# Kernel optimization log

Measured on AMD Instinct MI355X. Metric: run time of the kernel, lower is better.

The kernel has to match this reference:

```python
import jax, jax.numpy as jnp
import numpy as np

B, IN, H = 32768, 256, 256
CONCAT = IN + H

def _xavier(key, shape):
    fan_in, fan_out = shape
    limit = float(np.sqrt(6.0 / (fan_in + fan_out)))
    return jax.random.uniform(key, shape, jnp.float32, -limit, limit)

def setup_inputs() -> dict:
    key = jax.random.key(0)
    k = jax.random.split(key, 6)
    return {
        "x": jax.random.normal(k[0], (B, 1, IN), jnp.float32),
        "h_prev": jax.random.normal(k[1], (B, 1, H), jnp.float32),
        "wr": _xavier(k[2], (CONCAT, H)),
        "wz": _xavier(k[3], (CONCAT, H)),
        "whh": _xavier(k[4], (H, H)),
        "whx": _xavier(k[5], (IN, H)),
        "br": jnp.zeros((H,), jnp.float32),
        "bz": jnp.zeros((H,), jnp.float32),
        "bh": jnp.zeros((H,), jnp.float32),
    }

def reference(x, h_prev, wr, wz, whh, whx, br, bz, bh):
    # x: [B,1,IN], h_prev: [B,1,H]
    xc = jnp.concatenate([x, h_prev], axis=2)                  # [B,1,IN+H]
    r = jax.nn.sigmoid(jnp.matmul(xc, wr) + br)                # reset gate
    z = jax.nn.sigmoid(jnp.matmul(xc, wz) + bz)                # update gate
    g = jnp.tanh(jnp.matmul(r * h_prev, whh) + jnp.matmul(x, whx) + bh)
    h = (1 - z) * h_prev + z * g                               # gated blend
    return h
```

## Files before the change

### kernel.cpp

```cpp
#include <hip/hip_runtime.h>
#include <hip/hip_bf16.h>
#include <stdint.h>


typedef float  f32x4  __attribute__((ext_vector_type(4)));
typedef __bf16 bf16x8 __attribute__((ext_vector_type(8)));
typedef short  s16x8  __attribute__((ext_vector_type(8)));

#define B_TOT   32768
#define MT      64
#define WRZ_ELEMS (512*512)
#define WG_ELEMS  (256*512)

__device__ __forceinline__ unsigned short f2b(float f) {
    union { float f; unsigned int u; } v; v.f = f;
    unsigned int r = (v.u + 0x7FFFu + ((v.u >> 16) & 1u)) >> 16;
    return (unsigned short)r;
}
__device__ __forceinline__ float b2f(unsigned short b) {
    union { unsigned int u; float f; } v; v.u = ((unsigned int)b) << 16;
    return v.f;
}
__device__ __forceinline__ ushort2 pk2(float a, float b) {
    __hip_bfloat162 t = __float22bfloat162_rn(make_float2(a, b));
    union { __hip_bfloat162 h; ushort2 u; } c; c.h = t; return c.u;
}
__device__ __forceinline__ float sigmoid_f(float x) {
    return 1.0f / (1.0f + __expf(-x));
}
__device__ __forceinline__ float tanh_f(float x) {
    return 1.0f - 2.0f / (__expf(2.0f * x) + 1.0f);
}

__device__ __forceinline__ int lds_idx(int row, int col) {
    return row * 512 + ((((col >> 3) ^ (row & 7)) << 3) | (col & 7));
}

__global__ void prep_weights(const float* __restrict__ wr,
                             const float* __restrict__ wz,
                             const float* __restrict__ whh,
                             const float* __restrict__ whx,
                             unsigned short* __restrict__ wrz,
                             unsigned short* __restrict__ wg) {
    const int b = blockIdx.x;
    const int t = threadIdx.x;
    union { s16x8 v; unsigned short u[8]; } tmp;

    if (b < 128) {
        int w = b >> 4, ks = b & 15;
        int jn = t >> 6, l = t & 63;
        int kbase = ks * 32 + ((l >> 4) << 3);
        int n = 32 * w + ((jn & 1) << 4) + (l & 15);
        const float* src = (jn < 2) ? wr : wz;
        #pragma unroll
        for (int jj = 0; jj < 8; ++jj)
            tmp.u[jj] = f2b(src[(kbase + jj) * 256 + n]);
        *reinterpret_cast<s16x8*>(wrz + (size_t)w * 32768 + ks * 2048 + t * 8) = tmp.v;
    } else {
        int b2 = b - 128;
        int w = b2 >> 3, ksp = b2 & 7;
        int ksl = t >> 7, j = (t >> 6) & 1, l = t & 63;
        int ks = ksp * 2 + ksl;
        int kbase = ks * 32 + ((l >> 4) << 3);
        int n = 32 * w + (j << 4) + (l & 15);
        #pragma unroll
        for (int jj = 0; jj < 8; ++jj) {
            int k = kbase + jj;
            tmp.u[jj] = f2b((k < 256) ? whx[k * 256 + n] : whh[(k - 256) * 256 + n]);
        }
        *reinterpret_cast<s16x8*>(wg + (size_t)w * 16384 + ksp * 2048 + t * 8) = tmp.v;
    }
}

__global__ __launch_bounds__(512, 2)
void gru_fused(const float* __restrict__ x, const float* __restrict__ h,
               const unsigned short* __restrict__ wrz,
               const unsigned short* __restrict__ wg,
               const float* __restrict__ br, const float* __restrict__ bz,
               const float* __restrict__ bh, float* __restrict__ out) {
    __shared__ unsigned short xcA[64 * 512];

    const int tid  = threadIdx.x;
    const int lane = tid & 63;
    const int wv   = tid >> 6;
    const int m0   = lane & 15;
    const int q    = lane >> 4;
    const int rowBase = blockIdx.x * MT;

    float brv[2], bzv[2], bhv[2];
    #pragma unroll
    for (int j = 0; j < 2; ++j) {
        int col = 32 * wv + j * 16 + m0;
        brv[j] = br[col]; bzv[j] = bz[col]; bhv[j] = bh[col];
    }

    #pragma unroll
    for (int it = 0; it < 8; ++it) {
        int row = it * 8 + wv;
        size_t g = (size_t)(rowBase + row) * 256 + lane * 4;
        float4 xv = *reinterpret_cast<const float4*>(x + g);
        float4 hv = *reinterpret_cast<const float4*>(h + g);
        ushort2 x0 = pk2(xv.x, xv.y), x1 = pk2(xv.z, xv.w);
        ushort2 h0 = pk2(hv.x, hv.y), h1 = pk2(hv.z, hv.w);
        ushort4 xb = make_ushort4(x0.x, x0.y, x1.x, x1.y);
        ushort4 hb = make_ushort4(h0.x, h0.y, h1.x, h1.y);
        *reinterpret_cast<ushort4*>(&xcA[lds_idx(row, lane * 4)])       = xb;
        *reinterpret_cast<ushort4*>(&xcA[lds_idx(row, 256 + lane * 4)]) = hb;
    }

    const unsigned short* wrzP = wrz + (size_t)wv * 32768;
    const unsigned short* wgP  = wg  + (size_t)wv * 16384;

    s16x8 Bb[2][12];
    #pragma unroll
    for (int k2 = 0; k2 < 2; ++k2) {
        #pragma unroll
        for (int jn = 0; jn < 4; ++jn)
            Bb[0][k2 * 6 + jn] = *reinterpret_cast<const s16x8*>(
                wrzP + k2 * 2048 + jn * 512 + lane * 8);
        #pragma unroll
        for (int j = 0; j < 2; ++j)
            Bb[0][k2 * 6 + 4 + j] = *reinterpret_cast<const s16x8*>(
                wgP + k2 * 1024 + j * 512 + lane * 8);
    }

    __syncthreads();

    f32x4 rz[4][4];
    f32x4 gac[2][4];
    #pragma unroll
    for (int jn = 0; jn < 4; ++jn)
        #pragma unroll
        for (int mt = 0; mt < 4; ++mt)
            rz[jn][mt] = (f32x4){0.f, 0.f, 0.f, 0.f};
    #pragma unroll
    for (int j = 0; j < 2; ++j)
        #pragma unroll
        for (int mt = 0; mt < 4; ++mt)
            gac[j][mt] = (f32x4){0.f, 0.f, 0.f, 0.f};

    #pragma unroll
    for (int grp = 0; grp < 8; ++grp) {
        const int cur = grp & 1, nxt = cur ^ 1;
        if (grp < 7) {
            int gn = grp + 1;
            #pragma unroll
            for (int k2 = 0; k2 < 2; ++k2) {
                int ks = gn * 2 + k2;
                #pragma unroll
                for (int jn = 0; jn < 4; ++jn)
                    Bb[nxt][k2 * 6 + jn] = *reinterpret_cast<const s16x8*>(
                        wrzP + ks * 2048 + jn * 512 + lane * 8);
                if (gn < 4) {
                    #pragma unroll
                    for (int j = 0; j < 2; ++j)
                        Bb[nxt][k2 * 6 + 4 + j] = *reinterpret_cast<const s16x8*>(
                            wgP + ks * 1024 + j * 512 + lane * 8);
                }
            }
        }
        __builtin_amdgcn_sched_barrier(0);
        #pragma unroll
        for (int k2 = 0; k2 < 2; ++k2) {
            int ks = grp * 2 + k2;
            bf16x8 afr[4];
            #pragma unroll
            for (int mt = 0; mt < 4; ++mt) {
                int row = mt * 16 + m0;
                int idx = row * 512 + ((((ks << 2) | q) ^ (row & 7)) << 3);
                afr[mt] = __builtin_bit_cast(bf16x8,
                    *reinterpret_cast<const s16x8*>(&xcA[idx]));
            }
            #pragma unroll
            for (int jn = 0; jn < 4; ++jn) {
                bf16x8 bf = __builtin_bit_cast(bf16x8, Bb[cur][k2 * 6 + jn]);
                #pragma unroll
                for (int mt = 0; mt < 4; ++mt)
                    rz[jn][mt] = __builtin_amdgcn_mfma_f32_16x16x32_bf16(
                        afr[mt], bf, rz[jn][mt], 0, 0, 0);
            }
            if (grp < 4) {
                #pragma unroll
                for (int j = 0; j < 2; ++j) {
                    bf16x8 bf = __builtin_bit_cast(bf16x8, Bb[cur][k2 * 6 + 4 + j]);
                    #pragma unroll
                    for (int mt = 0; mt < 4; ++mt)
                        gac[j][mt] = __builtin_amdgcn_mfma_f32_16x16x32_bf16(
                            afr[mt], bf, gac[j][mt], 0, 0, 0);
                }
            }
        }
    }
    __syncthreads();

    s16x8 Tb[2][4];
    #pragma unroll
    for (int k2 = 0; k2 < 2; ++k2)
        #pragma unroll
        for (int j = 0; j < 2; ++j)
            Tb[0][k2 * 2 + j] = *reinterpret_cast<const s16x8*>(
                wgP + (8 + k2) * 1024 + j * 512 + lane * 8);

    #pragma unroll
    for (int j = 0; j < 2; ++j) {
        int col = 32 * wv + j * 16 + m0;
        #pragma unroll
        for (int mt = 0; mt < 4; ++mt) {
            #pragma unroll
            for (int rg = 0; rg < 4; ++rg) {
                int row = mt * 16 + q * 4 + rg;
                float hval = b2f(xcA[lds_idx(row, 256 + col)]);
                float rs = sigmoid_f(rz[j][mt][rg] + brv[j]);
                xcA[lds_idx(row, col)] = f2b(rs * hval);
                rz[j][mt][rg] = hval;
            }
        }
    }
    __syncthreads();

    #pragma unroll
    for (int tg = 0; tg < 4; ++tg) {
        const int cur = tg & 1, nxt = cur ^ 1;
        if (tg < 3) {
            #pragma unroll
            for (int k2 = 0; k2 < 2; ++k2)
                #pragma unroll
                for (int j = 0; j < 2; ++j)
                    Tb[nxt][k2 * 2 + j] = *reinterpret_cast<const s16x8*>(
                        wgP + (10 + tg * 2 + k2) * 1024 + j * 512 + lane * 8);
        }
        __builtin_amdgcn_sched_barrier(0);
        #pragma unroll
        for (int k2 = 0; k2 < 2; ++k2) {
            int kt = tg * 2 + k2;
            bf16x8 afr[4];
            #pragma unroll
            for (int mt = 0; mt < 4; ++mt) {
                int row = mt * 16 + m0;
                int idx = row * 512 + ((((kt << 2) | q) ^ (row & 7)) << 3);
                afr[mt] = __builtin_bit_cast(bf16x8,
                    *reinterpret_cast<const s16x8*>(&xcA[idx]));
            }
            #pragma unroll
            for (int j = 0; j < 2; ++j) {
                bf16x8 bf = __builtin_bit_cast(bf16x8, Tb[cur][k2 * 2 + j]);
                #pragma unroll
                for (int mt = 0; mt < 4; ++mt)
                    gac[j][mt] = __builtin_amdgcn_mfma_f32_16x16x32_bf16(
                        afr[mt], bf, gac[j][mt], 0, 0, 0);
            }
        }
    }

    #pragma unroll
    for (int j = 0; j < 2; ++j) {
        int col = 32 * wv + j * 16 + m0;
        #pragma unroll
        for (int mt = 0; mt < 4; ++mt) {
            #pragma unroll
            for (int rg = 0; rg < 4; ++rg) {
                int row = mt * 16 + q * 4 + rg;
                float zs = sigmoid_f(rz[2 + j][mt][rg] + bzv[j]);
                float gv = tanh_f(gac[j][mt][rg] + bhv[j]);
                float hval = rz[j][mt][rg];
                out[(size_t)(rowBase + row) * 256 + col] = hval + zs * (gv - hval);
            }
        }
    }
}

extern "C" void kernel_launch(void* const* d_in, const int* in_sizes, int n_in,
                              void* d_out, int out_size, void* d_ws, size_t ws_size,
                              hipStream_t stream) {
    const float* x   = (const float*)d_in[0];
    const float* h   = (const float*)d_in[1];
    const float* wr  = (const float*)d_in[2];
    const float* wz  = (const float*)d_in[3];
    const float* whh = (const float*)d_in[4];
    const float* whx = (const float*)d_in[5];
    const float* br  = (const float*)d_in[6];
    const float* bz  = (const float*)d_in[7];
    const float* bh  = (const float*)d_in[8];
    float* out = (float*)d_out;

    unsigned short* wrz = (unsigned short*)d_ws;
    unsigned short* wg  = wrz + WRZ_ELEMS;

    prep_weights<<<192, 256, 0, stream>>>(wr, wz, whh, whx, wrz, wg);
    gru_fused<<<B_TOT / MT, 512, 0, stream>>>(x, h, wrz, wg, br, bz, bh, out);
}
```

Measured before the change: 145.6 us.

## Stream activation tiles into LDS per k-group overlapped with MFMA compute

```diff
diff --git a/kernel.cpp b/kernel.cpp
--- a/kernel.cpp
+++ b/kernel.cpp
@@ -34,6 +34,13 @@
 
 __device__ __forceinline__ int lds_idx(int row, int col) {
     return row * 512 + ((((col >> 3) ^ (row & 7)) << 3) | (col & 7));
+}
+
+__device__ __forceinline__ void stash8(unsigned short* dst, float4 a, float4 b) {
+    union { ushort2 u2[4]; s16x8 v; } pk;
+    pk.u2[0] = pk2(a.x, a.y); pk.u2[1] = pk2(a.z, a.w);
+    pk.u2[2] = pk2(b.x, b.y); pk.u2[3] = pk2(b.z, b.w);
+    *reinterpret_cast<s16x8*>(dst) = pk.v;
 }
 
 __global__ void prep_weights(const float* __restrict__ wr,
@@ -72,7 +79,7 @@
     }
 }
 
-__global__ __launch_bounds__(512, 2)
+__global__ __launch_bounds__(512, 4)
 void gru_fused(const float* __restrict__ x, const float* __restrict__ h,
                const unsigned short* __restrict__ wrz,
                const unsigned short* __restrict__ wg,
@@ -94,22 +101,21 @@
         brv[j] = br[col]; bzv[j] = bz[col]; bhv[j] = bh[col];
     }
 
-    #pragma unroll
-    for (int it = 0; it < 8; ++it) {
-        int row = it * 8 + wv;
-        size_t g = (size_t)(rowBase + row) * 256 + lane * 4;
-        float4 xv = *reinterpret_cast<const float4*>(x + g);
-        float4 hv = *reinterpret_cast<const float4*>(h + g);
-        ushort2 x0 = pk2(xv.x, xv.y), x1 = pk2(xv.z, xv.w);
-        ushort2 h0 = pk2(hv.x, hv.y), h1 = pk2(hv.z, hv.w);
-        ushort4 xb = make_ushort4(x0.x, x0.y, x1.x, x1.y);
-        ushort4 hb = make_ushort4(h0.x, h0.y, h1.x, h1.y);
-        *reinterpret_cast<ushort4*>(&xcA[lds_idx(row, lane * 4)])       = xb;
-        *reinterpret_cast<ushort4*>(&xcA[lds_idx(row, 256 + lane * 4)]) = hb;
-    }
+    const int srow  = tid >> 3;
+    const int scol8 = (tid & 7) << 3;
+    const float* xrow = x + (size_t)(rowBase + srow) * 256 + scol8;
+    const float* hrow = h + (size_t)(rowBase + srow) * 256 + scol8;
 
     const unsigned short* wrzP = wrz + (size_t)wv * 32768;
     const unsigned short* wgP  = wg  + (size_t)wv * 16384;
+
+    float4 Sa[2], Sb[2];
+    {
+        const float4* p0 = reinterpret_cast<const float4*>(xrow);
+        Sa[0] = p0[0]; Sb[0] = p0[1];
+        const float4* p1 = reinterpret_cast<const float4*>(xrow + 64);
+        Sa[1] = p1[0]; Sb[1] = p1[1];
+    }
 
     s16x8 Bb[2][12];
     #pragma unroll
@@ -124,7 +130,11 @@
                 wgP + k2 * 1024 + j * 512 + lane * 8);
     }
 
-    __syncthreads();
+    stash8(&xcA[lds_idx(srow, scol8)], Sa[0], Sb[0]);
+    asm volatile("s_waitcnt lgkmcnt(0)" ::: "memory");
+    __builtin_amdgcn_sched_barrier(0);
+    __builtin_amdgcn_s_barrier();
+    __builtin_amdgcn_sched_barrier(0);
 
     f32x4 rz[4][4];
     f32x4 gac[2][4];
@@ -142,6 +152,12 @@
     #pragma unroll
     for (int grp = 0; grp < 8; ++grp) {
         const int cur = grp & 1, nxt = cur ^ 1;
+        if (grp < 6) {
+            const int s = grp + 2;
+            const float4* p = reinterpret_cast<const float4*>(
+                (s < 4) ? (xrow + 64 * s) : (hrow + 64 * (s - 4)));
+            Sa[grp & 1] = p[0]; Sb[grp & 1] = p[1];
+        }
         if (grp < 7) {
             int gn = grp + 1;
             #pragma unroll
@@ -189,6 +205,15 @@
                             afr[mt], bf, gac[j][mt], 0, 0, 0);
                 }
             }
+        }
+        __builtin_amdgcn_sched_barrier(0);
+        if (grp < 7) {
+            const int sb = (grp + 1) & 1;
+            stash8(&xcA[lds_idx(srow, 64 * (grp + 1) + scol8)], Sa[sb], Sb[sb]);
+            asm volatile("s_waitcnt lgkmcnt(0)" ::: "memory");
+            __builtin_amdgcn_sched_barrier(0);
+            __builtin_amdgcn_s_barrier();
+            __builtin_amdgcn_sched_barrier(0);
         }
     }
     __syncthreads();
```

Result: slower. 337.8 us (+132.0%).

## Halve row tile to 32, raise occupancy, drop register double-buffering of weights

Applied to the files above, without the earlier changes.

```diff
diff --git a/kernel.cpp b/kernel.cpp
--- a/kernel.cpp
+++ b/kernel.cpp
@@ -8,9 +8,8 @@
 typedef short  s16x8  __attribute__((ext_vector_type(8)));
 
 #define B_TOT   32768
-#define MT      64
+#define MT      32
 #define WRZ_ELEMS (512*512)
-#define WG_ELEMS  (256*512)
 
 __device__ __forceinline__ unsigned short f2b(float f) {
     union { float f; unsigned int u; } v; v.f = f;
@@ -72,13 +71,13 @@
     }
 }
 
-__global__ __launch_bounds__(512, 2)
+__global__ __launch_bounds__(512, 4)
 void gru_fused(const float* __restrict__ x, const float* __restrict__ h,
                const unsigned short* __restrict__ wrz,
                const unsigned short* __restrict__ wg,
                const float* __restrict__ br, const float* __restrict__ bz,
                const float* __restrict__ bh, float* __restrict__ out) {
-    __shared__ unsigned short xcA[64 * 512];
+    __shared__ unsigned short xcA[32 * 512];
 
     const int tid  = threadIdx.x;
     const int lane = tid & 63;
@@ -94,118 +93,89 @@
         brv[j] = br[col]; bzv[j] = bz[col]; bhv[j] = bh[col];
     }
 
-    #pragma unroll
-    for (int it = 0; it < 8; ++it) {
-        int row = it * 8 + wv;
-        size_t g = (size_t)(rowBase + row) * 256 + lane * 4;
-        float4 xv = *reinterpret_cast<const float4*>(x + g);
-        float4 hv = *reinterpret_cast<const float4*>(h + g);
-        ushort2 x0 = pk2(xv.x, xv.y), x1 = pk2(xv.z, xv.w);
-        ushort2 h0 = pk2(hv.x, hv.y), h1 = pk2(hv.z, hv.w);
-        ushort4 xb = make_ushort4(x0.x, x0.y, x1.x, x1.y);
-        ushort4 hb = make_ushort4(h0.x, h0.y, h1.x, h1.y);
-        *reinterpret_cast<ushort4*>(&xcA[lds_idx(row, lane * 4)])       = xb;
-        *reinterpret_cast<ushort4*>(&xcA[lds_idx(row, 256 + lane * 4)]) = hb;
+    {
+        const int srow = tid >> 4;
+        const int c4   = (tid & 15) << 2;
+        const float* xr = x + (size_t)(rowBase + srow) * 256 + c4;
+        const float* hr = h + (size_t)(rowBase + srow) * 256 + c4;
+        #pragma unroll
+        for (int u = 0; u < 4; ++u) {
+            float4 xv = *reinterpret_cast<const float4*>(xr + u * 64);
+            float4 hv = *reinterpret_cast<const float4*>(hr + u * 64);
+            ushort2 x0 = pk2(xv.x, xv.y), x1 = pk2(xv.z, xv.w);
+            ushort2 h0 = pk2(hv.x, hv.y), h1 = pk2(hv.z, hv.w);
+            ushort4 xb = make_ushort4(x0.x, x0.y, x1.x, x1.y);
+            ushort4 hb = make_ushort4(h0.x, h0.y, h1.x, h1.y);
+            *reinterpret_cast<ushort4*>(&xcA[lds_idx(srow, u * 64 + c4)])       = xb;
+            *reinterpret_cast<ushort4*>(&xcA[lds_idx(srow, 256 + u * 64 + c4)]) = hb;
+        }
     }
 
     const unsigned short* wrzP = wrz + (size_t)wv * 32768;
     const unsigned short* wgP  = wg  + (size_t)wv * 16384;
 
-    s16x8 Bb[2][12];
-    #pragma unroll
-    for (int k2 = 0; k2 < 2; ++k2) {
+    __syncthreads();
+
+    f32x4 rz[4][2];
+    f32x4 gac[2][2];
+    #pragma unroll
+    for (int jn = 0; jn < 4; ++jn)
+        #pragma unroll
+        for (int mt = 0; mt < 2; ++mt)
+            rz[jn][mt] = (f32x4){0.f, 0.f, 0.f, 0.f};
+    #pragma unroll
+    for (int j = 0; j < 2; ++j)
+        #pragma unroll
+        for (int mt = 0; mt < 2; ++mt)
+            gac[j][mt] = (f32x4){0.f, 0.f, 0.f, 0.f};
+
+    #pragma unroll
+    for (int ks = 0; ks < 16; ++ks) {
+        s16x8 Bf[4], Bg[2];
         #pragma unroll
         for (int jn = 0; jn < 4; ++jn)
-            Bb[0][k2 * 6 + jn] = *reinterpret_cast<const s16x8*>(
-                wrzP + k2 * 2048 + jn * 512 + lane * 8);
-        #pragma unroll
-        for (int j = 0; j < 2; ++j)
-            Bb[0][k2 * 6 + 4 + j] = *reinterpret_cast<const s16x8*>(
-                wgP + k2 * 1024 + j * 512 + lane * 8);
-    }
-
+            Bf[jn] = *reinterpret_cast<const s16x8*>(
+                wrzP + ks * 2048 + jn * 512 + lane * 8);
+        if (ks < 8) {
+            #pragma unroll
+            for (int j = 0; j < 2; ++j)
+                Bg[j] = *reinterpret_cast<const s16x8*>(
+                    wgP + ks * 1024 + j * 512 + lane * 8);
+        }
+        bf16x8 afr[2];
+        #pragma unroll
+        for (int mt = 0; mt < 2; ++mt) {
+            int row = mt * 16 + m0;
+            int idx = row * 512 + ((((ks << 2) | q) ^ (row & 7)) << 3);
+            afr[mt] = __builtin_bit_cast(bf16x8,
+                *reinterpret_cast<const s16x8*>(&xcA[idx]));
+        }
+        #pragma unroll
+        for (int jn = 0; jn < 4; ++jn) {
+            bf16x8 bf = __builtin_bit_cast(bf16x8, Bf[jn]);
+            #pragma unroll
+            for (int mt = 0; mt < 2; ++mt)
+                rz[jn][mt] = __builtin_amdgcn_mfma_f32_16x16x32_bf16(
+                    afr[mt], bf, rz[jn][mt], 0, 0, 0);
+        }
+        if (ks < 8) {
+            #pragma unroll
+            for (int j = 0; j < 2; ++j) {
+                bf16x8 bf = __builtin_bit_cast(bf16x8, Bg[j]);
+                #pragma unroll
+                for (int mt = 0; mt < 2; ++mt)
+                    gac[j][mt] = __builtin_amdgcn_mfma_f32_16x16x32_bf16(
+                        afr[mt], bf, gac[j][mt], 0, 0, 0);
+            }
+        }
+    }
     __syncthreads();
-
-    f32x4 rz[4][4];
-    f32x4 gac[2][4];
-    #pragma unroll
-    for (int jn = 0; jn < 4; ++jn)
-        #pragma unroll
-        for (int mt = 0; mt < 4; ++mt)
-            rz[jn][mt] = (f32x4){0.f, 0.f, 0.f, 0.f};
-    #pragma unroll
-    for (int j = 0; j < 2; ++j)
-        #pragma unroll
-        for (int mt = 0; mt < 4; ++mt)
-            gac[j][mt] = (f32x4){0.f, 0.f, 0.f, 0.f};
-
-    #pragma unroll
-    for (int grp = 0; grp < 8; ++grp) {
-        const int cur = grp & 1, nxt = cur ^ 1;
-        if (grp < 7) {
-            int gn = grp + 1;
-            #pragma unroll
-            for (int k2 = 0; k2 < 2; ++k2) {
-                int ks = gn * 2 + k2;
-                #pragma unroll
-                for (int jn = 0; jn < 4; ++jn)
-                    Bb[nxt][k2 * 6 + jn] = *reinterpret_cast<const s16x8*>(
-                        wrzP + ks * 2048 + jn * 512 + lane * 8);
-                if (gn < 4) {
-                    #pragma unroll
-                    for (int j = 0; j < 2; ++j)
-                        Bb[nxt][k2 * 6 + 4 + j] = *reinterpret_cast<const s16x8*>(
-                            wgP + ks * 1024 + j * 512 + lane * 8);
-                }
-            }
-        }
-        __builtin_amdgcn_sched_barrier(0);
-        #pragma unroll
-        for (int k2 = 0; k2 < 2; ++k2) {
-            int ks = grp * 2 + k2;
-            bf16x8 afr[4];
-            #pragma unroll
-            for (int mt = 0; mt < 4; ++mt) {
-                int row = mt * 16 + m0;
-                int idx = row * 512 + ((((ks << 2) | q) ^ (row & 7)) << 3);
-                afr[mt] = __builtin_bit_cast(bf16x8,
-                    *reinterpret_cast<const s16x8*>(&xcA[idx]));
-            }
-            #pragma unroll
-            for (int jn = 0; jn < 4; ++jn) {
-                bf16x8 bf = __builtin_bit_cast(bf16x8, Bb[cur][k2 * 6 + jn]);
-                #pragma unroll
-                for (int mt = 0; mt < 4; ++mt)
-                    rz[jn][mt] = __builtin_amdgcn_mfma_f32_16x16x32_bf16(
-                        afr[mt], bf, rz[jn][mt], 0, 0, 0);
-            }
-            if (grp < 4) {
-                #pragma unroll
-                for (int j = 0; j < 2; ++j) {
-                    bf16x8 bf = __builtin_bit_cast(bf16x8, Bb[cur][k2 * 6 + 4 + j]);
-                    #pragma unroll
-                    for (int mt = 0; mt < 4; ++mt)
-                        gac[j][mt] = __builtin_amdgcn_mfma_f32_16x16x32_bf16(
-                            afr[mt], bf, gac[j][mt], 0, 0, 0);
-                }
-            }
-        }
-    }
-    __syncthreads();
-
-    s16x8 Tb[2][4];
-    #pragma unroll
-    for (int k2 = 0; k2 < 2; ++k2)
-        #pragma unroll
-        for (int j = 0; j < 2; ++j)
-            Tb[0][k2 * 2 + j] = *reinterpret_cast<const s16x8*>(
-                wgP + (8 + k2) * 1024 + j * 512 + lane * 8);
 
     #pragma unroll
     for (int j = 0; j < 2; ++j) {
         int col = 32 * wv + j * 16 + m0;
         #pragma unroll
-        for (int mt = 0; mt < 4; ++mt) {
+        for (int mt = 0; mt < 2; ++mt) {
             #pragma unroll
             for (int rg = 0; rg < 4; ++rg) {
                 int row = mt * 16 + q * 4 + rg;
@@ -219,36 +189,27 @@
     __syncthreads();
 
     #pragma unroll
-    for (int tg = 0; tg < 4; ++tg) {
-        const int cur = tg & 1, nxt = cur ^ 1;
-        if (tg < 3) {
-            #pragma unroll
-            for (int k2 = 0; k2 < 2; ++k2)
-                #pragma unroll
-                for (int j = 0; j < 2; ++j)
-                    Tb[nxt][k2 * 2 + j] = *reinterpret_cast<const s16x8*>(
-                        wgP + (10 + tg * 2 + k2) * 1024 + j * 512 + lane * 8);
-        }
-        __builtin_amdgcn_sched_barrier(0);
-        #pragma unroll
-        for (int k2 = 0; k2 < 2; ++k2) {
-            int kt = tg * 2 + k2;
-            bf16x8 afr[4];
-            #pragma unroll
-            for (int mt = 0; mt < 4; ++mt) {
-                int row = mt * 16 + m0;
-                int idx = row * 512 + ((((kt << 2) | q) ^ (row & 7)) << 3);
-                afr[mt] = __builtin_bit_cast(bf16x8,
-                    *reinterpret_cast<const s16x8*>(&xcA[idx]));
-            }
-            #pragma unroll
-            for (int j = 0; j < 2; ++j) {
-                bf16x8 bf = __builtin_bit_cast(bf16x8, Tb[cur][k2 * 2 + j]);
-                #pragma unroll
-                for (int mt = 0; mt < 4; ++mt)
-                    gac[j][mt] = __builtin_amdgcn_mfma_f32_16x16x32_bf16(
-                        afr[mt], bf, gac[j][mt], 0, 0, 0);
-            }
+    for (int kt = 0; kt < 8; ++kt) {
+        s16x8 Tb[2];
+        #pragma unroll
+        for (int j = 0; j < 2; ++j)
+            Tb[j] = *reinterpret_cast<const s16x8*>(
+                wgP + (8 + kt) * 1024 + j * 512 + lane * 8);
+        bf16x8 afr[2];
+        #pragma unroll
+        for (int mt = 0; mt < 2; ++mt) {
+            int row = mt * 16 + m0;
+            int idx = row * 512 + ((((kt << 2) | q) ^ (row & 7)) << 3);
+            afr[mt] = __builtin_bit_cast(bf16x8,
+                *reinterpret_cast<const s16x8*>(&xcA[idx]));
+        }
+        #pragma unroll
+        for (int j = 0; j < 2; ++j) {
+            bf16x8 bf = __builtin_bit_cast(bf16x8, Tb[j]);
+            #pragma unroll
+            for (int mt = 0; mt < 2; ++mt)
+                gac[j][mt] = __builtin_amdgcn_mfma_f32_16x16x32_bf16(
+                    afr[mt], bf, gac[j][mt], 0, 0, 0);
         }
     }
 
@@ -256,7 +217,7 @@
     for (int j = 0; j < 2; ++j) {
         int col = 32 * wv + j * 16 + m0;
         #pragma unroll
-        for (int mt = 0; mt < 4; ++mt) {
+        for (int mt = 0; mt < 2; ++mt) {
             #pragma unroll
             for (int rg = 0; rg < 4; ++rg) {
                 int row = mt * 16 + q * 4 + rg;
```

New measurement: 152.4 us. 4.6% more time.
